# Kernel optimization log

Measured on AMD Instinct MI355X. Metric: run time of the kernel, lower is better.

Reference implementation:

```python
import jax, jax.numpy as jnp
import numpy as np

HIDDEN = 1024
N_HEAD = 16
HEAD_DIM = HIDDEN // N_HEAD


def setup_inputs() -> dict:
    key = jax.random.key(0)
    ks = jax.random.split(key, 11)
    B, S, D, H, E = 4, 1024, HIDDEN, N_HEAD, HEAD_DIM
    sc = 0.02
    return {
        "query": jax.random.normal(ks[0], (B, S, D), jnp.float32),
        "key": jax.random.normal(ks[1], (B, S, D), jnp.float32),
        "value": jax.random.normal(ks[2], (B, S, D), jnp.float32),
        # per-head projection weights stacked over heads (torch Linear: y = x @ W.T + b)
        "Wq": jax.random.normal(ks[3], (H, D, E), jnp.float32) * sc,
        "bq": jax.random.normal(ks[4], (H, E), jnp.float32) * sc,
        "Wk": jax.random.normal(ks[5], (H, D, E), jnp.float32) * sc,
        "bk": jax.random.normal(ks[6], (H, E), jnp.float32) * sc,
        "Wv": jax.random.normal(ks[7], (H, D, E), jnp.float32) * sc,
        "bv": jax.random.normal(ks[8], (H, E), jnp.float32) * sc,
        "Wo": jax.random.normal(ks[9], (D, D), jnp.float32) * sc,
        "bo": jax.random.normal(ks[10], (D,), jnp.float32) * sc,
    }


def reference(query, key, value, Wq, bq, Wk, bk, Wv, bv, Wo, bo):
    B, S, D = query.shape
    H, _, E = Wq.shape
    # per-head linear projections (vectorized over heads)
    q = jnp.einsum("bsd,hde->bhse", query, Wq) + bq[None, :, None, :]
    k = jnp.einsum("bsd,hde->bhse", key, Wk) + bk[None, :, None, :]
    v = jnp.einsum("bsd,hde->bhse", value, Wv) + bv[None, :, None, :]
    scale = jnp.sqrt(jnp.asarray(E, q.dtype))
    scores = jnp.einsum("bhse,bhte->bhst", q, k) / scale  # [B,H,S,S]
    attn = jax.nn.softmax(scores, axis=-1)  # dropout is identity in eval
    wv = jnp.einsum("bhst,bhte->bhse", attn, v)  # [B,H,S,E]
    # concat heads along feature dim (head h -> slice h*E:(h+1)*E)
    wv = wv.transpose(0, 2, 1, 3).reshape(B, S, H * E)
    out = wv @ Wo.T + bo  # final linear; output dropout identity in eval
    return out
```

## Files before the change

### kernel.cpp

```cpp
#include <hip/hip_runtime.h>

typedef unsigned short u16;
typedef unsigned int u32;
typedef __attribute__((ext_vector_type(8))) short bf16x8;
typedef __attribute__((ext_vector_type(4))) float f32x4;

#define B_SZ 4
#define S_SZ 1024
#define D_SZ 1024
#define H_SZ 16
#define E_SZ 64
#define M_SZ (B_SZ * S_SZ)

__device__ __forceinline__ u16 f2bf(float f) {
  union { float f; unsigned u; } x; x.f = f;
  unsigned r = (x.u + 0x7FFFu + ((x.u >> 16) & 1u)) >> 16;
  return (u16)r;
}

__device__ __forceinline__ u32 pack_bf16(float lo, float hi) {
  return (u32)f2bf(lo) | ((u32)f2bf(hi) << 16);
}

__device__ __forceinline__ void async16(const void* g, void* l) {
  __builtin_amdgcn_global_load_lds(
      (const __attribute__((address_space(1))) void*)g,
      (__attribute__((address_space(3))) void*)l, 16, 0, 0);
}

__device__ __forceinline__ f32x4 mfma16(bf16x8 a, bf16x8 b, f32x4 c) {
  return __builtin_amdgcn_mfma_f32_16x16x32_bf16(a, b, c, 0, 0, 0);
}

__global__ void cast3(const float* __restrict__ q, const float* __restrict__ k,
                      const float* __restrict__ v, u16* __restrict__ oq,
                      u16* __restrict__ ok, u16* __restrict__ ov) {
  int gid = blockIdx.x * 256 + threadIdx.x;
  int sel = gid >> 19;
  int i = (gid & ((1 << 19) - 1)) << 3;
  const float* in = sel == 0 ? q : (sel == 1 ? k : v);
  u16* out = sel == 0 ? oq : (sel == 1 ? ok : ov);
  float4 a = *(const float4*)(in + i);
  float4 b = *(const float4*)(in + i + 4);
  alignas(16) u16 r[8];
  r[0] = f2bf(a.x); r[1] = f2bf(a.y); r[2] = f2bf(a.z); r[3] = f2bf(a.w);
  r[4] = f2bf(b.x); r[5] = f2bf(b.y); r[6] = f2bf(b.z); r[7] = f2bf(b.w);
  *(uint4*)(out + i) = *(uint4*)r;
}

__global__ void cast_bf16_k(const float* __restrict__ in, u16* __restrict__ out, int n) {
  int i = (blockIdx.x * 256 + threadIdx.x) * 8;
  if (i >= n) return;
  float4 a = *(const float4*)(in + i);
  float4 b = *(const float4*)(in + i + 4);
  alignas(16) u16 r[8];
  r[0] = f2bf(a.x); r[1] = f2bf(a.y); r[2] = f2bf(a.z); r[3] = f2bf(a.w);
  r[4] = f2bf(b.x); r[5] = f2bf(b.y); r[6] = f2bf(b.z); r[7] = f2bf(b.w);
  *(uint4*)(out + i) = *(uint4*)r;
}

__global__ void transW3(const float* __restrict__ Wq, const float* __restrict__ Wk,
                        const float* __restrict__ Wv, u16* __restrict__ Tq,
                        u16* __restrict__ Tk, u16* __restrict__ Tv) {
  __shared__ float tile[64 * 68];
  const int wsel = blockIdx.x >> 8;
  const int bi = blockIdx.x & 255;
  const float* W = wsel == 0 ? Wq : (wsel == 1 ? Wk : Wv);
  u16* WT = wsel == 0 ? Tq : (wsel == 1 ? Tk : Tv);
  const int tid = threadIdx.x;
  const int h = bi >> 4;
  const int d0 = (bi & 15) << 6;
#pragma unroll
  for (int c = 0; c < 4; ++c) {
    const int dd = c * 16 + (tid >> 4);
    const int e4 = (tid & 15) << 2;
    float4 vq = *(const float4*)(W + (h << 16) + ((d0 + dd) << 6) + e4);
    *(float4*)(tile + dd * 68 + e4) = vq;
  }
  __syncthreads();
  {
    const int e = tid >> 2;
    const int dc = (tid & 3) << 4;
    alignas(16) u16 outv[16];
#pragma unroll
    for (int i = 0; i < 16; ++i) outv[i] = f2bf(tile[(dc + i) * 68 + e]);
    u16* dst = WT + (((size_t)(h << 6) + e) << 10) + d0 + dc;
    *(uint4*)(dst) = *(uint4*)outv;
    *(uint4*)(dst + 8) = *(uint4*)(outv + 8);
  }
}

__device__ __forceinline__ void gemm_core(const u16* __restrict__ A,
                                          const u16* __restrict__ BT,
                                          const float* __restrict__ bias,
                                          void* __restrict__ Cout,
                                          float scale, int mode, int bi) {
  __shared__ u16 Al[128 * 64];
  __shared__ u16 Bl[128 * 64];
  const int tid = threadIdx.x;
  const int wave = tid >> 6;
  const int lane = tid & 63;
  const int l15 = lane & 15, lq = lane >> 4;
  const int bm = bi >> 3;
  const int bn = bi & 7;
  const int row0 = bm << 7, col0 = bn << 7;
  const int wr = ((wave >> 1) & 1) << 6;
  const int wc = (wave & 1) << 6;

  f32x4 acc[4][4];
#pragma unroll
  for (int m = 0; m < 4; ++m)
#pragma unroll
    for (int n = 0; n < 4; ++n) acc[m][n] = (f32x4)0.0f;

  for (int k0 = 0; k0 < 1024; k0 += 64) {
    __syncthreads();
#pragma unroll
    for (int c = 0; c < 4; ++c) {
      const int x = c * 4096 + tid * 16;
      const int g = x ^ (((x >> 7) & 7) << 4);
      const int row = g >> 7;
      const int cb = g & 127;
      const u16* ga = A + (size_t)(row0 + row) * 1024 + k0 + (cb >> 1);
      const u16* gb = BT + (size_t)(col0 + row) * 1024 + k0 + (cb >> 1);
      async16(ga, (char*)Al + c * 4096 + (wave << 10));
      async16(gb, (char*)Bl + c * 4096 + (wave << 10));
    }
    __syncthreads();

    bf16x8 af[4][2], bfr[4][2];
#pragma unroll
    for (int m = 0; m < 4; ++m)
#pragma unroll
      for (int kf = 0; kf < 2; ++kf) {
        int r = wr + m * 16 + l15;
        int byte = ((r << 7) + kf * 64 + lq * 16) ^ ((r & 7) << 4);
        af[m][kf] = *(const bf16x8*)((const char*)Al + byte);
      }
#pragma unroll
    for (int n = 0; n < 4; ++n)
#pragma unroll
      for (int kf = 0; kf < 2; ++kf) {
        int r = wc + n * 16 + l15;
        int byte = ((r << 7) + kf * 64 + lq * 16) ^ ((r & 7) << 4);
        bfr[n][kf] = *(const bf16x8*)((const char*)Bl + byte);
      }
#pragma unroll
    for (int kf = 0; kf < 2; ++kf)
#pragma unroll
      for (int m = 0; m < 4; ++m)
#pragma unroll
        for (int n = 0; n < 4; ++n)
          acc[m][n] = mfma16(af[m][kf], bfr[n][kf], acc[m][n]);
  }

#pragma unroll
  for (int m = 0; m < 4; ++m)
#pragma unroll
    for (int n = 0; n < 4; ++n) {
      int col = col0 + wc + n * 16 + l15;
      float bv = bias[col];
      int rowb = row0 + wr + m * 16 + lq * 4;
      if (mode == 2) {
        alignas(8) u16 r4[4];
#pragma unroll
        for (int j = 0; j < 4; ++j) r4[j] = f2bf((acc[m][n][j] + bv) * scale);
        *(uint2*)((u16*)Cout + (size_t)col * 4096 + rowb) = *(uint2*)r4;
      } else if (mode == 1) {
#pragma unroll
        for (int j = 0; j < 4; ++j)
          ((u16*)Cout)[(size_t)(rowb + j) * 1024 + col] = f2bf((acc[m][n][j] + bv) * scale);
      } else {
#pragma unroll
        for (int j = 0; j < 4; ++j)
          ((float*)Cout)[(size_t)(rowb + j) * 1024 + col] = (acc[m][n][j] + bv) * scale;
      }
    }
}

__global__ __launch_bounds__(256)
void gemm3(const u16* __restrict__ qb, const u16* __restrict__ kb, const u16* __restrict__ vb,
           const u16* __restrict__ Tq, const u16* __restrict__ Tk, const u16* __restrict__ Tv,
           const float* __restrict__ bq, const float* __restrict__ bk, const float* __restrict__ bv,
           u16* __restrict__ Qp, u16* __restrict__ Kp, u16* __restrict__ VpT) {
  const int g = blockIdx.x >> 8;
  const int bi = blockIdx.x & 255;
  const u16* A = g == 0 ? qb : (g == 1 ? kb : vb);
  const u16* BT = g == 0 ? Tq : (g == 1 ? Tk : Tv);
  const float* bias = g == 0 ? bq : (g == 1 ? bk : bv);
  void* out = g == 0 ? (void*)Qp : (g == 1 ? (void*)Kp : (void*)VpT);
  gemm_core(A, BT, bias, out, g == 0 ? 0.125f : 1.0f, g == 2 ? 2 : 1, bi);
}

__global__ __launch_bounds__(256)
void gemmO(const u16* __restrict__ A, const u16* __restrict__ BT,
           const float* __restrict__ bias, float* __restrict__ out) {
  gemm_core(A, BT, bias, out, 1.0f, 0, blockIdx.x);
}

__global__ __launch_bounds__(256)
void attn(const u16* __restrict__ Qp, const u16* __restrict__ Kp,
          const u16* __restrict__ VpT, u16* __restrict__ Ow) {
  __shared__ alignas(16) u16 Kl[2][64 * 64];
  __shared__ alignas(16) u16 VTl[2][64 * 64];
  __shared__ alignas(16) u16 Pl[4][16 * 64];
  const int tid = threadIdx.x;
  const int wave = tid >> 6;
  const int lane = tid & 63;
  const int l15 = lane & 15, lq = lane >> 4;
  const int qt = blockIdx.x & 15;
  const int bh = blockIdx.x >> 4;
  const int b = bh >> 4, h = bh & 15;
  const size_t bS = (size_t)b * S_SZ;

  const int xs0 = tid * 16, xs1 = 4096 + tid * 16;
  const int r0 = xs0 >> 7, r1 = xs1 >> 7;
  const int c0 = ((xs0 & 127) ^ (((xs0 >> 7) & 7) << 4)) >> 1;
  const int c1 = ((xs1 & 127) ^ (((xs1 >> 7) & 7) << 4)) >> 1;
  const u16* Kb0 = Kp + ((bS + r0) << 10) + h * 64 + c0;
  const u16* Kb1 = Kp + ((bS + r1) << 10) + h * 64 + c1;
  const u16* Vb0 = VpT + (size_t)(h * 64 + r0) * 4096 + bS + c0;
  const u16* Vb1 = VpT + (size_t)(h * 64 + r1) * 4096 + bS + c1;

  bf16x8 aq[2];
  {
    const u16* qptr = Qp + ((bS + qt * 64 + wave * 16 + l15) << 10) + h * 64 + lq * 8;
    aq[0] = *(const bf16x8*)(qptr);
    aq[1] = *(const bf16x8*)(qptr + 32);
  }

  f32x4 o[4];
#pragma unroll
  for (int n = 0; n < 4; ++n) o[n] = (f32x4)0.0f;
  float m_run = -1e30f;
  float l_run = 0.f;
  u16* Pw = Pl[wave];

  async16(Kb0, (char*)Kl[0] + xs0);
  async16(Kb1, (char*)Kl[0] + xs1);
  async16(Vb0, (char*)VTl[0] + xs0);
  async16(Vb1, (char*)VTl[0] + xs1);
  __syncthreads();

  int buf = 0;
  for (int t0 = 0; t0 < S_SZ; t0 += 64) {
    if (t0 + 64 < S_SZ) {
      const int tn = t0 + 64;
      async16(Kb0 + ((size_t)tn << 10), (char*)Kl[buf ^ 1] + xs0);
      async16(Kb1 + ((size_t)tn << 10), (char*)Kl[buf ^ 1] + xs1);
      async16(Vb0 + tn, (char*)VTl[buf ^ 1] + xs0);
      async16(Vb1 + tn, (char*)VTl[buf ^ 1] + xs1);
    }

    f32x4 s[4];
#pragma unroll
    for (int n = 0; n < 4; ++n) s[n] = (f32x4)0.0f;
#pragma unroll
    for (int n = 0; n < 4; ++n)
#pragma unroll
      for (int kf = 0; kf < 2; ++kf) {
        int r = n * 16 + l15;
        int byte = ((r << 7) + kf * 64 + lq * 16) ^ ((r & 7) << 4);
        bf16x8 bk = *(const bf16x8*)((const char*)Kl[buf] + byte);
        s[n] = mfma16(bk, aq[kf], s[n]);
      }

    float mx = s[0][0];
#pragma unroll
    for (int n = 0; n < 4; ++n)
#pragma unroll
      for (int j = 0; j < 4; ++j) mx = fmaxf(mx, s[n][j]);
    mx = fmaxf(mx, __shfl_xor(mx, 16, 64));
    mx = fmaxf(mx, __shfl_xor(mx, 32, 64));

    if (__any(mx > m_run + 8.0f)) {
      float mn = fmaxf(m_run, mx);
      float alpha = __expf(m_run - mn);
      m_run = mn;
      l_run *= alpha;
      float a0 = __shfl(alpha, lq * 4 + 0, 64);
      float a1 = __shfl(alpha, lq * 4 + 1, 64);
      float a2 = __shfl(alpha, lq * 4 + 2, 64);
      float a3 = __shfl(alpha, lq * 4 + 3, 64);
#pragma unroll
      for (int n = 0; n < 4; ++n) {
        o[n][0] *= a0; o[n][1] *= a1; o[n][2] *= a2; o[n][3] *= a3;
      }
    }

    float rs = 0.f;
#pragma unroll
    for (int n = 0; n < 4; ++n) {
      float p0 = __expf(s[n][0] - m_run);
      float p1 = __expf(s[n][1] - m_run);
      float p2 = __expf(s[n][2] - m_run);
      float p3 = __expf(s[n][3] - m_run);
      rs += (p0 + p1) + (p2 + p3);
      u32 lo = pack_bf16(p0, p1);
      u32 hi = pack_bf16(p2, p3);
      int byte = (l15 << 7) + (((n * 32 + lq * 8)) ^ ((l15 & 7) << 4));
      uint2 wv; wv.x = lo; wv.y = hi;
      *(uint2*)((char*)Pw + byte) = wv;
    }
    rs += __shfl_xor(rs, 16, 64);
    rs += __shfl_xor(rs, 32, 64);
    l_run += rs;

#pragma unroll
    for (int kf = 0; kf < 2; ++kf) {
      int pbyte = (l15 << 7) + ((kf * 64 + lq * 16) ^ ((l15 & 7) << 4));
      bf16x8 pa = *(const bf16x8*)((const char*)Pw + pbyte);
#pragma unroll
      for (int n = 0; n < 4; ++n) {
        int vr = n * 16 + l15;
        int byte = ((vr << 7) + kf * 64 + lq * 16) ^ ((vr & 7) << 4);
        bf16x8 bv = *(const bf16x8*)((const char*)VTl[buf] + byte);
        o[n] = mfma16(pa, bv, o[n]);
      }
    }

    __syncthreads();
    buf ^= 1;
  }

  float li0 = __shfl(l_run, lq * 4 + 0, 64);
  float li1 = __shfl(l_run, lq * 4 + 1, 64);
  float li2 = __shfl(l_run, lq * 4 + 2, 64);
  float li3 = __shfl(l_run, lq * 4 + 3, 64);
  float inv0 = 1.0f / li0, inv1 = 1.0f / li1, inv2 = 1.0f / li2, inv3 = 1.0f / li3;
#pragma unroll
  for (int n = 0; n < 4; ++n) {
    float vals[4] = {o[n][0] * inv0, o[n][1] * inv1, o[n][2] * inv2, o[n][3] * inv3};
#pragma unroll
    for (int j = 0; j < 4; ++j) {
      int row = qt * 64 + wave * 16 + lq * 4 + j;
      int col = h * 64 + n * 16 + l15;
      Ow[((bS + row) << 10) + col] = f2bf(vals[j]);
    }
  }
}

extern "C" void kernel_launch(void* const* d_in, const int* in_sizes, int n_in,
                              void* d_out, int out_size, void* d_ws, size_t ws_size,
                              hipStream_t stream) {
  const float* q  = (const float*)d_in[0];
  const float* k  = (const float*)d_in[1];
  const float* v  = (const float*)d_in[2];
  const float* Wq = (const float*)d_in[3];
  const float* bq = (const float*)d_in[4];
  const float* Wk = (const float*)d_in[5];
  const float* bk = (const float*)d_in[6];
  const float* Wv = (const float*)d_in[7];
  const float* bv = (const float*)d_in[8];
  const float* Wo = (const float*)d_in[9];
  const float* bo = (const float*)d_in[10];

  char* w = (char*)d_ws;
  const size_t MB = 1u << 20;
  u16* qb  = (u16*)(w + 0 * MB);
  u16* kb  = (u16*)(w + 8 * MB);
  u16* vb  = (u16*)(w + 16 * MB);
  u16* WqT = (u16*)(w + 24 * MB);
  u16* WkT = (u16*)(w + 26 * MB);
  u16* WvT = (u16*)(w + 28 * MB);
  u16* Wob = (u16*)(w + 30 * MB);
  u16* Qp  = (u16*)(w + 32 * MB);
  u16* Kp  = (u16*)(w + 40 * MB);
  u16* VpT = (u16*)(w + 48 * MB);
  u16* wvb = (u16*)(w + 56 * MB);

  const int nW = H_SZ * D_SZ * E_SZ;

  cast3<<<6144, 256, 0, stream>>>(q, k, v, qb, kb, vb);
  cast_bf16_k<<<nW / 2048, 256, 0, stream>>>(Wo, Wob, nW);
  transW3<<<768, 256, 0, stream>>>(Wq, Wk, Wv, WqT, WkT, WvT);

  gemm3<<<768, 256, 0, stream>>>(qb, kb, vb, WqT, WkT, WvT, bq, bk, bv, Qp, Kp, VpT);

  attn<<<B_SZ * H_SZ * (S_SZ / 64), 256, 0, stream>>>(Qp, Kp, VpT, wvb);

  gemmO<<<256, 256, 0, stream>>>(wvb, Wob, bo, (float*)d_out);
}
```

Before: 134.0 us.

## Merge cast kernels, vectorize GEMM epilogues, 8-wave output GEMM, MFMA priority hints

Folds the Wo cast into the q/k/v cast kernel to drop one launch. In the Q/K projection GEMM it swaps the MFMA operand order so each lane holds contiguous columns, allowing packed 8-byte bf16 stores and float4 bias loads. It replaces the output GEMM with a 512-thread, 8-wave variant that writes float4 results. It also adds s_setprio around the attention MFMA sections to favor matrix issue. These touch several kernels at once and add code complexity; the 8-wave GEMM halves per-wave work and may shift occupancy.

Result: faster. 127.1 us (-5.1%).

```diff
diff --git a/kernel.cpp b/kernel.cpp
--- a/kernel.cpp
+++ b/kernel.cpp
@@ -32,25 +32,24 @@
   return __builtin_amdgcn_mfma_f32_16x16x32_bf16(a, b, c, 0, 0, 0);
 }
 
-__global__ void cast3(const float* __restrict__ q, const float* __restrict__ k,
-                      const float* __restrict__ v, u16* __restrict__ oq,
-                      u16* __restrict__ ok, u16* __restrict__ ov) {
+__global__ void cast4(const float* __restrict__ q, const float* __restrict__ k,
+                      const float* __restrict__ v, const float* __restrict__ Wo,
+                      u16* __restrict__ oq, u16* __restrict__ ok,
+                      u16* __restrict__ ov, u16* __restrict__ oWo) {
   int gid = blockIdx.x * 256 + threadIdx.x;
-  int sel = gid >> 19;
-  int i = (gid & ((1 << 19) - 1)) << 3;
-  const float* in = sel == 0 ? q : (sel == 1 ? k : v);
-  u16* out = sel == 0 ? oq : (sel == 1 ? ok : ov);
-  float4 a = *(const float4*)(in + i);
-  float4 b = *(const float4*)(in + i + 4);
-  alignas(16) u16 r[8];
-  r[0] = f2bf(a.x); r[1] = f2bf(a.y); r[2] = f2bf(a.z); r[3] = f2bf(a.w);
-  r[4] = f2bf(b.x); r[5] = f2bf(b.y); r[6] = f2bf(b.z); r[7] = f2bf(b.w);
-  *(uint4*)(out + i) = *(uint4*)r;
-}
-
-__global__ void cast_bf16_k(const float* __restrict__ in, u16* __restrict__ out, int n) {
-  int i = (blockIdx.x * 256 + threadIdx.x) * 8;
-  if (i >= n) return;
+  const float* in;
+  u16* out;
+  int i;
+  if (gid < (3 << 19)) {
+    int sel = gid >> 19;
+    i = (gid & ((1 << 19) - 1)) << 3;
+    in = sel == 0 ? q : (sel == 1 ? k : v);
+    out = sel == 0 ? oq : (sel == 1 ? ok : ov);
+  } else {
+    i = (gid - (3 << 19)) << 3;
+    in = Wo;
+    out = oWo;
+  }
   float4 a = *(const float4*)(in + i);
   float4 b = *(const float4*)(in + i + 4);
   alignas(16) u16 r[8];
@@ -90,13 +89,21 @@
   }
 }
 
-__device__ __forceinline__ void gemm_core(const u16* __restrict__ A,
-                                          const u16* __restrict__ BT,
-                                          const float* __restrict__ bias,
-                                          void* __restrict__ Cout,
-                                          float scale, int mode, int bi) {
+__global__ __launch_bounds__(256)
+void gemm3(const u16* __restrict__ qb, const u16* __restrict__ kb, const u16* __restrict__ vb,
+           const u16* __restrict__ Tq, const u16* __restrict__ Tk, const u16* __restrict__ Tv,
+           const float* __restrict__ bq, const float* __restrict__ bk, const float* __restrict__ bv,
+           u16* __restrict__ Qp, u16* __restrict__ Kp, u16* __restrict__ VpT) {
   __shared__ u16 Al[128 * 64];
   __shared__ u16 Bl[128 * 64];
+  const int g = blockIdx.x >> 8;
+  const int bi = blockIdx.x & 255;
+  const u16* A = g == 0 ? qb : (g == 1 ? kb : vb);
+  const u16* BT = g == 0 ? Tq : (g == 1 ? Tk : Tv);
+  const float* bias = g == 0 ? bq : (g == 1 ? bk : bv);
+  u16* Cout = g == 0 ? Qp : (g == 1 ? Kp : VpT);
+  const float scale = g == 0 ? 0.125f : 1.0f;
+
   const int tid = threadIdx.x;
   const int wave = tid >> 6;
   const int lane = tid & 63;
@@ -118,13 +125,13 @@
 #pragma unroll
     for (int c = 0; c < 4; ++c) {
       const int x = c * 4096 + tid * 16;
-      const int g = x ^ (((x >> 7) & 7) << 4);
-      const int row = g >> 7;
-      const int cb = g & 127;
+      const int gx = x ^ (((x >> 7) & 7) << 4);
+      const int row = gx >> 7;
+      const int cb = gx & 127;
       const u16* ga = A + (size_t)(row0 + row) * 1024 + k0 + (cb >> 1);
       const u16* gb = BT + (size_t)(col0 + row) * 1024 + k0 + (cb >> 1);
-      async16(ga, (char*)Al + c * 4096 + (wave << 10));
-      async16(gb, (char*)Bl + c * 4096 + (wave << 10));
+      async16(ga, (char*)Al + x);
+      async16(gb, (char*)Bl + x);
     }
     __syncthreads();
 
@@ -145,57 +152,141 @@
         int byte = ((r << 7) + kf * 64 + lq * 16) ^ ((r & 7) << 4);
         bfr[n][kf] = *(const bf16x8*)((const char*)Bl + byte);
       }
+    if (g == 2) {
+#pragma unroll
+      for (int kf = 0; kf < 2; ++kf)
+#pragma unroll
+        for (int m = 0; m < 4; ++m)
+#pragma unroll
+          for (int n = 0; n < 4; ++n)
+            acc[m][n] = mfma16(af[m][kf], bfr[n][kf], acc[m][n]);
+    } else {
+#pragma unroll
+      for (int kf = 0; kf < 2; ++kf)
+#pragma unroll
+        for (int m = 0; m < 4; ++m)
+#pragma unroll
+          for (int n = 0; n < 4; ++n)
+            acc[m][n] = mfma16(bfr[n][kf], af[m][kf], acc[m][n]);
+    }
+  }
+
+  if (g == 2) {
+#pragma unroll
+    for (int m = 0; m < 4; ++m)
+#pragma unroll
+      for (int n = 0; n < 4; ++n) {
+        int col = col0 + wc + n * 16 + l15;
+        float bv = bias[col];
+        int rowb = row0 + wr + m * 16 + lq * 4;
+        alignas(8) u16 r4[4];
+#pragma unroll
+        for (int j = 0; j < 4; ++j) r4[j] = f2bf(acc[m][n][j] + bv);
+        *(uint2*)(Cout + (size_t)col * 4096 + rowb) = *(uint2*)r4;
+      }
+  } else {
+    float4 b4[4];
+#pragma unroll
+    for (int n = 0; n < 4; ++n)
+      b4[n] = *(const float4*)(bias + col0 + wc + n * 16 + lq * 4);
+#pragma unroll
+    for (int m = 0; m < 4; ++m) {
+      int row = row0 + wr + m * 16 + l15;
+#pragma unroll
+      for (int n = 0; n < 4; ++n) {
+        int colbase = col0 + wc + n * 16 + lq * 4;
+        u32 lo = pack_bf16((acc[m][n][0] + b4[n].x) * scale,
+                           (acc[m][n][1] + b4[n].y) * scale);
+        u32 hi = pack_bf16((acc[m][n][2] + b4[n].z) * scale,
+                           (acc[m][n][3] + b4[n].w) * scale);
+        uint2 wv; wv.x = lo; wv.y = hi;
+        *(uint2*)(Cout + (size_t)row * 1024 + colbase) = wv;
+      }
+    }
+  }
+}
+
+__global__ __launch_bounds__(512)
+void gemmO8(const u16* __restrict__ A, const u16* __restrict__ BT,
+            const float* __restrict__ bias, float* __restrict__ out) {
+  __shared__ u16 Al[128 * 64];
+  __shared__ u16 Bl[128 * 64];
+  const int tid = threadIdx.x;
+  const int wave = tid >> 6;
+  const int lane = tid & 63;
+  const int l15 = lane & 15, lq = lane >> 4;
+  const int bi = blockIdx.x;
+  const int bm = bi >> 3;
+  const int bn = bi & 7;
+  const int row0 = bm << 7, col0 = bn << 7;
+  const int wr = (wave >> 1) << 5;
+  const int wc = (wave & 1) << 6;
+
+  f32x4 acc[2][4];
+#pragma unroll
+  for (int m = 0; m < 2; ++m)
+#pragma unroll
+    for (int n = 0; n < 4; ++n) acc[m][n] = (f32x4)0.0f;
+
+  for (int k0 = 0; k0 < 1024; k0 += 64) {
+    __syncthreads();
+#pragma unroll
+    for (int c = 0; c < 2; ++c) {
+      const int x = c * 8192 + tid * 16;
+      const int gx = x ^ (((x >> 7) & 7) << 4);
+      const int row = gx >> 7;
+      const int cb = gx & 127;
+      const u16* ga = A + (size_t)(row0 + row) * 1024 + k0 + (cb >> 1);
+      const u16* gb = BT + (size_t)(col0 + row) * 1024 + k0 + (cb >> 1);
+      async16(ga, (char*)Al + x);
+      async16(gb, (char*)Bl + x);
+    }
+    __syncthreads();
+
+    bf16x8 af[2][2], bfr[4][2];
+#pragma unroll
+    for (int m = 0; m < 2; ++m)
+#pragma unroll
+      for (int kf = 0; kf < 2; ++kf) {
+        int r = wr + m * 16 + l15;
+        int byte = ((r << 7) + kf * 64 + lq * 16) ^ ((r & 7) << 4);
+        af[m][kf] = *(const bf16x8*)((const char*)Al + byte);
+      }
+#pragma unroll
+    for (int n = 0; n < 4; ++n)
+#pragma unroll
+      for (int kf = 0; kf < 2; ++kf) {
+        int r = wc + n * 16 + l15;
+        int byte = ((r << 7) + kf * 64 + lq * 16) ^ ((r & 7) << 4);
+        bfr[n][kf] = *(const bf16x8*)((const char*)Bl + byte);
+      }
 #pragma unroll
     for (int kf = 0; kf < 2; ++kf)
 #pragma unroll
-      for (int m = 0; m < 4; ++m)
+      for (int m = 0; m < 2; ++m)
 #pragma unroll
         for (int n = 0; n < 4; ++n)
-          acc[m][n] = mfma16(af[m][kf], bfr[n][kf], acc[m][n]);
-  }
-
-#pragma unroll
-  for (int m = 0; m < 4; ++m)
+          acc[m][n] = mfma16(bfr[n][kf], af[m][kf], acc[m][n]);
+  }
+
+  float4 b4[4];
+#pragma unroll
+  for (int n = 0; n < 4; ++n)
+    b4[n] = *(const float4*)(bias + col0 + wc + n * 16 + lq * 4);
+#pragma unroll
+  for (int m = 0; m < 2; ++m) {
+    int row = row0 + wr + m * 16 + l15;
 #pragma unroll
     for (int n = 0; n < 4; ++n) {
-      int col = col0 + wc + n * 16 + l15;
-      float bv = bias[col];
-      int rowb = row0 + wr + m * 16 + lq * 4;
-      if (mode == 2) {
-        alignas(8) u16 r4[4];
-#pragma unroll
-        for (int j = 0; j < 4; ++j) r4[j] = f2bf((acc[m][n][j] + bv) * scale);
-        *(uint2*)((u16*)Cout + (size_t)col * 4096 + rowb) = *(uint2*)r4;
-      } else if (mode == 1) {
-#pragma unroll
-        for (int j = 0; j < 4; ++j)
-          ((u16*)Cout)[(size_t)(rowb + j) * 1024 + col] = f2bf((acc[m][n][j] + bv) * scale);
-      } else {
-#pragma unroll
-        for (int j = 0; j < 4; ++j)
-          ((float*)Cout)[(size_t)(rowb + j) * 1024 + col] = (acc[m][n][j] + bv) * scale;
-      }
-    }
-}
-
-__global__ __launch_bounds__(256)
-void gemm3(const u16* __restrict__ qb, const u16* __restrict__ kb, const u16* __restrict__ vb,
-           const u16* __restrict__ Tq, const u16* __restrict__ Tk, const u16* __restrict__ Tv,
-           const float* __restrict__ bq, const float* __restrict__ bk, const float* __restrict__ bv,
-           u16* __restrict__ Qp, u16* __restrict__ Kp, u16* __restrict__ VpT) {
-  const int g = blockIdx.x >> 8;
-  const int bi = blockIdx.x & 255;
-  const u16* A = g == 0 ? qb : (g == 1 ? kb : vb);
-  const u16* BT = g == 0 ? Tq : (g == 1 ? Tk : Tv);
-  const float* bias = g == 0 ? bq : (g == 1 ? bk : bv);
-  void* out = g == 0 ? (void*)Qp : (g == 1 ? (void*)Kp : (void*)VpT);
-  gemm_core(A, BT, bias, out, g == 0 ? 0.125f : 1.0f, g == 2 ? 2 : 1, bi);
-}
-
-__global__ __launch_bounds__(256)
-void gemmO(const u16* __restrict__ A, const u16* __restrict__ BT,
-           const float* __restrict__ bias, float* __restrict__ out) {
-  gemm_core(A, BT, bias, out, 1.0f, 0, blockIdx.x);
+      int colbase = col0 + wc + n * 16 + lq * 4;
+      float4 v;
+      v.x = acc[m][n][0] + b4[n].x;
+      v.y = acc[m][n][1] + b4[n].y;
+      v.z = acc[m][n][2] + b4[n].z;
+      v.w = acc[m][n][3] + b4[n].w;
+      *(float4*)(out + (size_t)row * 1024 + colbase) = v;
+    }
+  }
 }
 
 __global__ __launch_bounds__(256)
@@ -255,6 +346,7 @@
     f32x4 s[4];
 #pragma unroll
     for (int n = 0; n < 4; ++n) s[n] = (f32x4)0.0f;
+    __builtin_amdgcn_s_setprio(1);
 #pragma unroll
     for (int n = 0; n < 4; ++n)
 #pragma unroll
@@ -264,6 +356,7 @@
         bf16x8 bk = *(const bf16x8*)((const char*)Kl[buf] + byte);
         s[n] = mfma16(bk, aq[kf], s[n]);
       }
+    __builtin_amdgcn_s_setprio(0);
 
     float mx = s[0][0];
 #pragma unroll
@@ -306,6 +399,7 @@
     rs += __shfl_xor(rs, 32, 64);
     l_run += rs;
 
+    __builtin_amdgcn_s_setprio(1);
 #pragma unroll
     for (int kf = 0; kf < 2; ++kf) {
       int pbyte = (l15 << 7) + ((kf * 64 + lq * 16) ^ ((l15 & 7) << 4));
@@ -318,6 +412,7 @@
         o[n] = mfma16(pa, bv, o[n]);
       }
     }
+    __builtin_amdgcn_s_setprio(0);
 
     __syncthreads();
     buf ^= 1;
@@ -369,15 +464,12 @@
   u16* VpT = (u16*)(w + 48 * MB);
   u16* wvb = (u16*)(w + 56 * MB);
 
-  const int nW = H_SZ * D_SZ * E_SZ;
-
-  cast3<<<6144, 256, 0, stream>>>(q, k, v, qb, kb, vb);
-  cast_bf16_k<<<nW / 2048, 256, 0, stream>>>(Wo, Wob, nW);
+  cast4<<<6656, 256, 0, stream>>>(q, k, v, Wo, qb, kb, vb, Wob);
   transW3<<<768, 256, 0, stream>>>(Wq, Wk, Wv, WqT, WkT, WvT);
 
   gemm3<<<768, 256, 0, stream>>>(qb, kb, vb, WqT, WkT, WvT, bq, bk, bv, Qp, Kp, VpT);
 
   attn<<<B_SZ * H_SZ * (S_SZ / 64), 256, 0, stream>>>(Qp, Kp, VpT, wvb);
 
-  gemmO<<<256, 256, 0, stream>>>(wvb, Wob, bo, (float*)d_out);
-}
+  gemmO8<<<256, 512, 0, stream>>>(wvb, Wob, bo, (float*)d_out);
+}
```
